# Performance work log

Measured on AMD Instinct MI355X. Metric: run time of the kernel, lower is better.

The kernel has to match this reference:

```python
import jax, jax.numpy as jnp
import numpy as np

RADIUS = 0.2
N_POINT = 1024   # FPS centroids
N_SAMPLE = 64    # ball-query neighbors


def swish(x):
    return x * jax.nn.sigmoid(x)


def farthest_point_sample(xyz, npoint):
    # xyz: [B, N, 3] -> [B, npoint] int32 indices (deterministic: start = arange(B) % N)
    B, N, _ = xyz.shape
    batch = jnp.arange(B)

    def step(carry, _):
        distance, farthest = carry
        centroid = xyz[batch, farthest][:, None, :]            # [B,1,3]
        dist = jnp.sum((xyz - centroid) ** 2, axis=-1)          # [B,N]
        distance = jnp.minimum(distance, dist)
        nxt = jnp.argmax(distance, axis=-1).astype(jnp.int32)
        return (distance, nxt), farthest

    init = (jnp.full((B, N), 1e10, dtype=xyz.dtype),
            (jnp.arange(B, dtype=jnp.int32) % N))
    _, idx = jax.lax.scan(step, init, None, length=npoint)      # [npoint, B]
    return idx.T                                                # [B, npoint]


def square_distance(src, dst):
    # src [B,S,3], dst [B,N,3] -> [B,S,N]
    return (jnp.sum(src ** 2, -1)[:, :, None]
            + jnp.sum(dst ** 2, -1)[:, None, :]
            - 2.0 * jnp.einsum('bsc,bnc->bsn', src, dst))


def query_ball_point(radius, nsample, xyz, new_xyz):
    # xyz [B,N,3], new_xyz [B,S,3] -> [B,S,nsample] int32
    N = xyz.shape[1]
    sqrdists = square_distance(new_xyz, xyz)                     # [B,S,N]
    arange_n = jnp.arange(N, dtype=jnp.int32)
    group_idx = jnp.where(sqrdists > radius ** 2, N, arange_n[None, None, :])
    group_idx = jnp.sort(group_idx, axis=-1)[:, :, :nsample]     # [B,S,K]
    first = group_idx[:, :, :1]
    return jnp.where(group_idx == N, first, group_idx).astype(jnp.int32)


def index_points(points, idx):
    # points [B,N,C], idx [B,...] -> [B,...,C]
    return jax.vmap(lambda p, i: p[i])(points, idx)


def setup_inputs() -> dict:
    key = jax.random.key(0)
    k1, k2, k3, k4 = jax.random.split(key, 4)
    B, N, D = 4, 16384, 256
    c_in = D + 3  # 259
    xyz = jax.random.normal(k1, (B, 3, N), dtype=jnp.float32)
    points = jax.random.normal(k2, (B, D, N), dtype=jnp.float32)
    w1 = jax.random.normal(k3, (512, c_in), dtype=jnp.float32) / np.sqrt(c_in)
    b1 = jnp.zeros((512,), dtype=jnp.float32)
    w2 = jax.random.normal(k4, (512, 512), dtype=jnp.float32) / np.sqrt(512)
    b2 = jnp.zeros((512,), dtype=jnp.float32)
    return {"xyz": xyz, "points": points, "w1": w1, "b1": b1, "w2": w2, "b2": b2}


def reference(xyz, points, w1, b1, w2, b2):
    x = jnp.transpose(xyz, (0, 2, 1))        # [B,N,3]
    p = jnp.transpose(points, (0, 2, 1))     # [B,N,D]

    fps_idx = farthest_point_sample(x, N_POINT)                  # [B,S]
    new_xyz = index_points(x, fps_idx)                           # [B,S,3]
    idx = query_ball_point(RADIUS, N_SAMPLE, x, new_xyz)         # [B,S,K]
    grouped_xyz = index_points(x, idx)                           # [B,S,K,3]
    grouped_norm = grouped_xyz - new_xyz[:, :, None, :]
    grouped_pts = index_points(p, idx)                           # [B,S,K,D]
    feat = jnp.concatenate([grouped_norm, grouped_pts], axis=-1) # [B,S,K,3+D]

    h = jnp.transpose(feat, (0, 3, 2, 1))                        # [B,C,K,S]
    # 1x1 convs (patch_size=1) == per-position channel GEMM
    h = swish(jnp.einsum('bcks,oc->boks', h, w1) + b1[None, :, None, None])
    h = swish(jnp.einsum('bcks,oc->boks', h, w2) + b2[None, :, None, None])
    return jnp.mean(h, axis=2)                                   # [B,512,S]
```

## Files before the change

kernel.cpp:

```cpp
#include <hip/hip_runtime.h>
#include <hip/hip_bf16.h>
#include <stdint.h>

#define BB 4
#define NN 16384
#define SS 1024
#define KSAMP 64
#define DD 256
#define CIN 259
#define HH 512
#define R2C 0.04f

#define OFF_PTS  0ull
#define OFF_Q    33554432ull
#define OFF_W1P  33816576ull
#define OFF_W2P  34111488ull
#define OFF_CX   34635776ull
#define OFF_CY   34652160ull
#define OFF_CZ   34668544ull
#define OFF_BIDX 34684928ull

typedef __attribute__((ext_vector_type(8))) short bf16x8;
typedef __attribute__((ext_vector_type(4))) short bf16x4;
typedef __attribute__((ext_vector_type(4))) float f32x4;

__device__ __forceinline__ unsigned short f2bf(float f) {
    unsigned u = __float_as_uint(f);
    u = u + 0x7fffu + ((u >> 16) & 1u);
    return (unsigned short)(u >> 16);
}

__global__ __launch_bounds__(1024) void k_prep(const float* __restrict__ xyz,
                                               const float* __restrict__ pts,
                                               const float* __restrict__ w1,
                                               const float* __restrict__ w2,
                                               unsigned char* __restrict__ ws)
{
    __shared__ __align__(16) unsigned char smem[64 * 264 * 2];
    const int blk = blockIdx.x;
    const int t   = threadIdx.x;

    if (blk < 4) {
        const int b = blk;
        const float* xb = xyz + (size_t)b * 3 * NN;
        float x[16], y[16], z[16], d[16];
        const int base = t * 16;
        const float4* xv = (const float4*)(xb + base);
        const float4* yv = (const float4*)(xb + NN + base);
        const float4* zv = (const float4*)(xb + 2 * NN + base);
#pragma unroll
        for (int i = 0; i < 4; i++) {
            float4 a = xv[i]; x[4*i]=a.x; x[4*i+1]=a.y; x[4*i+2]=a.z; x[4*i+3]=a.w;
            float4 c = yv[i]; y[4*i]=c.x; y[4*i+1]=c.y; y[4*i+2]=c.z; y[4*i+3]=c.w;
            float4 e = zv[i]; z[4*i]=e.x; z[4*i+1]=e.y; z[4*i+2]=e.z; z[4*i+3]=e.w;
        }
#pragma unroll
        for (int i = 0; i < 16; i++) d[i] = 1e10f;

        float* sC    = (float*)smem;
        float* sWMax = (float*)smem + 4;
        int*   sWin  = (int*)((float*)smem + 20);
        float* cxs = (float*)(ws + OFF_CX);
        float* cys = (float*)(ws + OFF_CY);
        float* czs = (float*)(ws + OFF_CZ);

        if (t == (b >> 4)) {
#pragma unroll
            for (int k = 0; k < 16; k++)
                if ((b & 15) == k) { sC[0] = x[k]; sC[1] = y[k]; sC[2] = z[k]; }
        }
        __syncthreads();

        for (int it = 0; it < SS; ++it) {
            const float cx = sC[0], cy = sC[1], cz = sC[2];
            if (t == 0) {
                cxs[(b << 10) + it] = cx;
                cys[(b << 10) + it] = cy;
                czs[(b << 10) + it] = cz;
                *sWin = 0x7fffffff;
            }
            if (it == SS - 1) break;

            float bl = -1.0f;
#pragma unroll
            for (int k = 0; k < 16; k++) {
                float dx = __fsub_rn(x[k], cx);
                float dy = __fsub_rn(y[k], cy);
                float dz = __fsub_rn(z[k], cz);
                float s  = __fadd_rn(__fadd_rn(__fmul_rn(dx, dx), __fmul_rn(dy, dy)),
                                     __fmul_rn(dz, dz));
                float nd = fminf(d[k], s);
                d[k] = nd;
                bl = fmaxf(bl, nd);
            }
            float bm = bl;
#pragma unroll
            for (int off = 32; off; off >>= 1) bm = fmaxf(bm, __shfl_xor(bm, off));
            if ((t & 63) == 0) sWMax[t >> 6] = bm;
            __syncthreads();

            float gm = sWMax[0];
#pragma unroll
            for (int wv = 1; wv < 16; wv++) gm = fmaxf(gm, sWMax[wv]);

            if (bl == gm) {
                int cand = 0x7fffffff;
#pragma unroll
                for (int k = 15; k >= 0; k--) if (d[k] == gm) cand = base + k;
                atomicMin(sWin, cand);
            }
            __syncthreads();
            const int w = *sWin;
            if (t == (w >> 4)) {
                const int wk = w & 15;
#pragma unroll
                for (int k = 0; k < 16; k++)
                    if (wk == k) { sC[0] = x[k]; sC[1] = y[k]; sC[2] = z[k]; }
            }
            __syncthreads();
        }
    } else if (blk < 1028) {
        const int tb = blk - 4;
        const int b  = tb >> 8;
        const int n0 = (tb & 255) << 6;
        unsigned short* sT = (unsigned short*)smem;
        const int tn = t & 63, tc = t >> 6;
        for (int cc = tc; cc < 256; cc += 16) {
            float v = pts[((size_t)(b * 256 + cc)) * NN + n0 + tn];
            sT[tn * 264 + cc] = f2bf(v);
        }
        __syncthreads();
        unsigned short* ptsT = (unsigned short*)(ws + OFF_PTS);
        const int r = t >> 4, part = t & 15;
        size_t ob = (((size_t)b * NN) + n0 + r) * 256 + part * 16;
        bf16x8* dst = (bf16x8*)(ptsT + ob);
        const bf16x8* src = (const bf16x8*)(sT + r * 264 + part * 16);
        dst[0] = src[0];
        dst[1] = src[1];
    } else if (blk < 1092) {
        const int qb = blk - 1028;
        const int b = qb >> 4;
        const int n = ((qb & 15) << 10) + t;
        const float* xb = xyz + (size_t)b * 3 * NN;
        float X = xb[n], Y = xb[NN + n], Z = xb[2 * NN + n];
        float q = __fadd_rn(__fadd_rn(__fmul_rn(X, X), __fmul_rn(Y, Y)), __fmul_rn(Z, Z));
        ((float*)(ws + OFF_Q))[b * NN + n] = q;
    } else if (blk == 1092) {
        unsigned short* w1p = (unsigned short*)(ws + OFF_W1P);
        for (int e = t; e < 32 * 9 * 64 * 8; e += 1024) {
            int j = e & 7, lane = (e >> 3) & 63, rest = e >> 9;
            int kt = rest % 9, nt = rest / 9;
            int kk = kt * 32 + 4 * (lane >> 4) + (j & 3) + 16 * (j >> 2);
            int o  = nt * 16 + (lane & 15);
            float v = 0.f;
            if (kk < CIN) {
                int c = (kk < 256) ? (kk + 3) : (kk - 256);
                v = w1[o * CIN + c];
            }
            w1p[e] = f2bf(v);
        }
    } else if (blk == 1093) {
        unsigned short* w2p = (unsigned short*)(ws + OFF_W2P);
        for (int e = t; e < 32 * 16 * 64 * 8; e += 1024) {
            int j = e & 7, lane = (e >> 3) & 63, rest = e >> 9;
            int kt = rest & 15, nt = rest >> 4;
            int kk = kt * 32 + 4 * (lane >> 4) + (j & 3) + 16 * (j >> 2);
            int o  = nt * 16 + (lane & 15);
            w2p[e] = f2bf(w2[o * 512 + kk]);
        }
    }
}

__global__ __launch_bounds__(256) void k_ball(const float* __restrict__ xyz,
                                              unsigned char* __restrict__ ws)
{
    const int s    = (blockIdx.x << 2) + (threadIdx.x >> 6);
    const int lane = threadIdx.x & 63;
    const int b    = s >> 10;
    const float* Q  = (const float*)(ws + OFF_Q) + b * NN;
    const float cx = ((const float*)(ws + OFF_CX))[s];
    const float cy = ((const float*)(ws + OFF_CY))[s];
    const float cz = ((const float*)(ws + OFF_CZ))[s];
    const float qc = __fadd_rn(__fadd_rn(__fmul_rn(cx, cx), __fmul_rn(cy, cy)),
                               __fmul_rn(cz, cz));
    const float* xb = xyz + (size_t)b * 3 * NN;
    int* gi = (int*)(ws + OFF_BIDX) + s * 64;

    int collected = 0;
    int first = -1;
    for (int c = 0; c < 256; c++) {
        const int n = (c << 6) + lane;
        float px = xb[n], py = xb[NN + n], pz = xb[2 * NN + n], qj = Q[n];
        float dot = __fadd_rn(__fadd_rn(__fmul_rn(cx, px), __fmul_rn(cy, py)),
                              __fmul_rn(cz, pz));
        float r = __fsub_rn(__fadd_rn(qc, qj), __fmul_rn(2.0f, dot));
        bool valid = !(r > R2C);
        unsigned long long m = __ballot(valid);
        if (m) {
            if (first < 0) first = (c << 6) + __builtin_ctzll(m);
            int rank = __popcll(m & ((1ull << lane) - 1ull));
            int slot = collected + rank;
            if (valid && slot < 64) gi[slot] = n;
            collected += __popcll(m);
            if (collected >= 64) break;
        }
    }
    if (collected < 64) {
        for (int k = collected + lane; k < 64; k += 64) gi[k] = first;
    }
}

__global__ __launch_bounds__(512) void k_mlp(const float* __restrict__ xyz,
                                             const float* __restrict__ b1,
                                             const float* __restrict__ b2,
                                             const unsigned char* __restrict__ ws,
                                             float* __restrict__ out)
{
    __shared__ __align__(16) unsigned short sFeat[64 * 296];
    __shared__ __align__(16) unsigned short sH1[64 * 520];
    __shared__ int sIdx[64];

    const int sblk = blockIdx.x;
    const int b = sblk >> 10, sq = sblk & 1023;
    const int t = threadIdx.x;

    const int* gi = (const int*)(ws + OFF_BIDX) + sblk * 64;
    if (t < 64) sIdx[t] = gi[t];
    __syncthreads();

    {
        const unsigned short* ptsT = (const unsigned short*)(ws + OFF_PTS);
        const int k = t >> 3, part = t & 7;
        const int n = sIdx[k];
        const bf16x8* src = (const bf16x8*)(ptsT + (((size_t)b * NN + n) * 256 + part * 32));
        bf16x8* dst = (bf16x8*)(sFeat + k * 296 + part * 32);
#pragma unroll
        for (int j = 0; j < 4; j++) dst[j] = src[j];
    }
    if (t < 64) {
        const int n = sIdx[t];
        const float* xb = xyz + (size_t)b * 3 * NN;
        const float cx = ((const float*)(ws + OFF_CX))[sblk];
        const float cy = ((const float*)(ws + OFF_CY))[sblk];
        const float cz = ((const float*)(ws + OFF_CZ))[sblk];
        sFeat[t * 296 + 256] = f2bf(__fsub_rn(xb[n], cx));
        sFeat[t * 296 + 257] = f2bf(__fsub_rn(xb[NN + n], cy));
        sFeat[t * 296 + 258] = f2bf(__fsub_rn(xb[2 * NN + n], cz));
#pragma unroll
        for (int c = 259; c < 288; c++) sFeat[t * 296 + c] = 0;
    }
    __syncthreads();

    const int wv = t >> 6, lane = t & 63;
    const int l15 = lane & 15, g = lane >> 4;

    f32x4 acc[4][4];
#pragma unroll
    for (int i = 0; i < 4; i++)
#pragma unroll
        for (int j = 0; j < 4; j++) acc[i][j] = (f32x4){0.f, 0.f, 0.f, 0.f};

    const bf16x8* w1v = (const bf16x8*)(ws + OFF_W1P);
    for (int kt = 0; kt < 9; kt++) {
        bf16x8 af[4];
#pragma unroll
        for (int mt = 0; mt < 4; mt++) {
            const unsigned short* p = sFeat + (mt * 16 + l15) * 296 + kt * 32 + 4 * g;
            bf16x4 lo = *(const bf16x4*)p;
            bf16x4 hi = *(const bf16x4*)(p + 16);
            af[mt] = __builtin_shufflevector(lo, hi, 0, 1, 2, 3, 4, 5, 6, 7);
        }
        bf16x8 bfr[4];
#pragma unroll
        for (int nti = 0; nti < 4; nti++)
            bfr[nti] = w1v[((wv * 4 + nti) * 9 + kt) * 64 + lane];
#pragma unroll
        for (int mt = 0; mt < 4; mt++)
#pragma unroll
            for (int nti = 0; nti < 4; nti++)
                acc[mt][nti] = __builtin_amdgcn_mfma_f32_16x16x32_bf16(
                    af[mt], bfr[nti], acc[mt][nti], 0, 0, 0);
    }
#pragma unroll
    for (int mt = 0; mt < 4; mt++)
#pragma unroll
        for (int nti = 0; nti < 4; nti++) {
            const int o = (wv * 4 + nti) * 16 + l15;
            const float bias = b1[o];
#pragma unroll
            for (int r = 0; r < 4; r++) {
                float v = acc[mt][nti][r] + bias;
                float sw = v / (1.f + __expf(-v));
                sH1[(mt * 16 + g * 4 + r) * 520 + o] = f2bf(sw);
            }
        }
    __syncthreads();

#pragma unroll
    for (int i = 0; i < 4; i++)
#pragma unroll
        for (int j = 0; j < 4; j++) acc[i][j] = (f32x4){0.f, 0.f, 0.f, 0.f};

    const bf16x8* w2v = (const bf16x8*)(ws + OFF_W2P);
    for (int kt = 0; kt < 16; kt++) {
        bf16x8 af[4];
#pragma unroll
        for (int mt = 0; mt < 4; mt++) {
            const unsigned short* p = sH1 + (mt * 16 + l15) * 520 + kt * 32 + 4 * g;
            bf16x4 lo = *(const bf16x4*)p;
            bf16x4 hi = *(const bf16x4*)(p + 16);
            af[mt] = __builtin_shufflevector(lo, hi, 0, 1, 2, 3, 4, 5, 6, 7);
        }
        bf16x8 bfr[4];
#pragma unroll
        for (int nti = 0; nti < 4; nti++)
            bfr[nti] = w2v[((wv * 4 + nti) * 16 + kt) * 64 + lane];
#pragma unroll
        for (int mt = 0; mt < 4; mt++)
#pragma unroll
            for (int nti = 0; nti < 4; nti++)
                acc[mt][nti] = __builtin_amdgcn_mfma_f32_16x16x32_bf16(
                    af[mt], bfr[nti], acc[mt][nti], 0, 0, 0);
    }
#pragma unroll
    for (int nti = 0; nti < 4; nti++) {
        float tot = 0.f;
        const int o = (wv * 4 + nti) * 16 + l15;
        const float bias = b2[o];
#pragma unroll
        for (int mt = 0; mt < 4; mt++) {
#pragma unroll
            for (int r = 0; r < 4; r++) {
                float v = acc[mt][nti][r] + bias;
                tot += v / (1.f + __expf(-v));
            }
        }
        tot += __shfl_xor(tot, 16);
        tot += __shfl_xor(tot, 32);
        if (lane < 16) {
            const int oo = (wv * 4 + nti) * 16 + lane;
            out[((size_t)b * 512 + oo) * 1024 + sq] = tot * 0.015625f;
        }
    }
}

extern "C" void kernel_launch(void* const* d_in, const int* in_sizes, int n_in,
                              void* d_out, int out_size, void* d_ws, size_t ws_size,
                              hipStream_t stream)
{
    const float* xyz = (const float*)d_in[0];
    const float* pts = (const float*)d_in[1];
    const float* w1  = (const float*)d_in[2];
    const float* b1  = (const float*)d_in[3];
    const float* w2  = (const float*)d_in[4];
    const float* b2  = (const float*)d_in[5];
    float* out = (float*)d_out;
    unsigned char* ws = (unsigned char*)d_ws;

    k_prep<<<1094, 1024, 0, stream>>>(xyz, pts, w1, w2, ws);
    k_ball<<<1024, 256, 0, stream>>>(xyz, ws);
    k_mlp<<<4096, 512, 0, stream>>>(xyz, b1, b2, ws, out);
}
```

Measured before the change: 1.901 ms.

## Cut FPS barriers using packed max-index keys and fewer threads

The farthest-point-sampling loop now packs the distance and inverted index into a 64-bit key and reduces it with wavefront shuffles, which needs one block barrier per iteration instead of three. A double-buffered shared slot lets that single barrier suffice, and every thread reads the winning centroid straight from global memory. The prep kernel drops to 512 threads so each thread covers 32 points, shrinking the cross-wave reduction to 8 waves. The other prep roles are adjusted to the new thread count. The trade-off is more registers per thread and a dependent global load on each serial FPS iteration.

```diff
diff --git a/kernel.cpp b/kernel.cpp
--- a/kernel.cpp
+++ b/kernel.cpp
@@ -30,11 +30,11 @@
     return (unsigned short)(u >> 16);
 }
 
-__global__ __launch_bounds__(1024) void k_prep(const float* __restrict__ xyz,
-                                               const float* __restrict__ pts,
-                                               const float* __restrict__ w1,
-                                               const float* __restrict__ w2,
-                                               unsigned char* __restrict__ ws)
+__global__ __launch_bounds__(512) void k_prep(const float* __restrict__ xyz,
+                                              const float* __restrict__ pts,
+                                              const float* __restrict__ w1,
+                                              const float* __restrict__ w2,
+                                              unsigned char* __restrict__ ws)
 {
     __shared__ __align__(16) unsigned char smem[64 * 264 * 2];
     const int blk = blockIdx.x;
@@ -43,47 +43,40 @@
     if (blk < 4) {
         const int b = blk;
         const float* xb = xyz + (size_t)b * 3 * NN;
-        float x[16], y[16], z[16], d[16];
-        const int base = t * 16;
+        float x[32], y[32], z[32], d[32];
+        const int base = t * 32;
         const float4* xv = (const float4*)(xb + base);
         const float4* yv = (const float4*)(xb + NN + base);
         const float4* zv = (const float4*)(xb + 2 * NN + base);
 #pragma unroll
-        for (int i = 0; i < 4; i++) {
+        for (int i = 0; i < 8; i++) {
             float4 a = xv[i]; x[4*i]=a.x; x[4*i+1]=a.y; x[4*i+2]=a.z; x[4*i+3]=a.w;
             float4 c = yv[i]; y[4*i]=c.x; y[4*i+1]=c.y; y[4*i+2]=c.z; y[4*i+3]=c.w;
             float4 e = zv[i]; z[4*i]=e.x; z[4*i+1]=e.y; z[4*i+2]=e.z; z[4*i+3]=e.w;
         }
 #pragma unroll
-        for (int i = 0; i < 16; i++) d[i] = 1e10f;
-
-        float* sC    = (float*)smem;
-        float* sWMax = (float*)smem + 4;
-        int*   sWin  = (int*)((float*)smem + 20);
+        for (int i = 0; i < 32; i++) d[i] = 1e10f;
+
+        unsigned long long* sK = (unsigned long long*)smem;
         float* cxs = (float*)(ws + OFF_CX);
         float* cys = (float*)(ws + OFF_CY);
         float* czs = (float*)(ws + OFF_CZ);
 
-        if (t == (b >> 4)) {
-#pragma unroll
-            for (int k = 0; k < 16; k++)
-                if ((b & 15) == k) { sC[0] = x[k]; sC[1] = y[k]; sC[2] = z[k]; }
-        }
-        __syncthreads();
+        const int wv = t >> 6, lane = t & 63;
+        float cx = xb[b], cy = xb[NN + b], cz = xb[2 * NN + b];
 
         for (int it = 0; it < SS; ++it) {
-            const float cx = sC[0], cy = sC[1], cz = sC[2];
             if (t == 0) {
                 cxs[(b << 10) + it] = cx;
                 cys[(b << 10) + it] = cy;
                 czs[(b << 10) + it] = cz;
-                *sWin = 0x7fffffff;
             }
             if (it == SS - 1) break;
 
             float bl = -1.0f;
-#pragma unroll
-            for (int k = 0; k < 16; k++) {
+            int   bi = 0;
+#pragma unroll
+            for (int k = 0; k < 32; k++) {
                 float dx = __fsub_rn(x[k], cx);
                 float dy = __fsub_rn(y[k], cy);
                 float dz = __fsub_rn(z[k], cz);
@@ -91,63 +84,63 @@
                                      __fmul_rn(dz, dz));
                 float nd = fminf(d[k], s);
                 d[k] = nd;
-                bl = fmaxf(bl, nd);
-            }
-            float bm = bl;
-#pragma unroll
-            for (int off = 32; off; off >>= 1) bm = fmaxf(bm, __shfl_xor(bm, off));
-            if ((t & 63) == 0) sWMax[t >> 6] = bm;
+                if (nd > bl) { bl = nd; bi = base + k; }
+            }
+            unsigned long long key =
+                ((unsigned long long)__float_as_uint(bl) << 32) |
+                (unsigned)(0xFFFFFFFFu - (unsigned)bi);
+#pragma unroll
+            for (int off = 1; off < 64; off <<= 1) {
+                unsigned long long o = __shfl_xor(key, off);
+                if (o > key) key = o;
+            }
+            if (lane == 0) sK[((it & 1) << 3) + wv] = key;
             __syncthreads();
 
-            float gm = sWMax[0];
-#pragma unroll
-            for (int wv = 1; wv < 16; wv++) gm = fmaxf(gm, sWMax[wv]);
-
-            if (bl == gm) {
-                int cand = 0x7fffffff;
-#pragma unroll
-                for (int k = 15; k >= 0; k--) if (d[k] == gm) cand = base + k;
-                atomicMin(sWin, cand);
-            }
-            __syncthreads();
-            const int w = *sWin;
-            if (t == (w >> 4)) {
-                const int wk = w & 15;
-#pragma unroll
-                for (int k = 0; k < 16; k++)
-                    if (wk == k) { sC[0] = x[k]; sC[1] = y[k]; sC[2] = z[k]; }
-            }
-            __syncthreads();
+            unsigned long long gk = sK[((it & 1) << 3) + (lane & 7)];
+#pragma unroll
+            for (int off = 1; off < 8; off <<= 1) {
+                unsigned long long o = __shfl_xor(gk, off);
+                if (o > gk) gk = o;
+            }
+            const int widx = (int)(0xFFFFFFFFu - (unsigned)gk);
+            cx = xb[widx]; cy = xb[NN + widx]; cz = xb[2 * NN + widx];
         }
     } else if (blk < 1028) {
         const int tb = blk - 4;
         const int b  = tb >> 8;
         const int n0 = (tb & 255) << 6;
         unsigned short* sT = (unsigned short*)smem;
-        const int tn = t & 63, tc = t >> 6;
-        for (int cc = tc; cc < 256; cc += 16) {
+        const int tn = t & 63, tc0 = t >> 6;
+        for (int cc = tc0; cc < 256; cc += 8) {
             float v = pts[((size_t)(b * 256 + cc)) * NN + n0 + tn];
             sT[tn * 264 + cc] = f2bf(v);
         }
         __syncthreads();
         unsigned short* ptsT = (unsigned short*)(ws + OFF_PTS);
-        const int r = t >> 4, part = t & 15;
-        size_t ob = (((size_t)b * NN) + n0 + r) * 256 + part * 16;
+        const int r = t >> 3, part = t & 7;
+        size_t ob = (((size_t)b * NN) + n0 + r) * 256 + part * 32;
         bf16x8* dst = (bf16x8*)(ptsT + ob);
-        const bf16x8* src = (const bf16x8*)(sT + r * 264 + part * 16);
+        const bf16x8* src = (const bf16x8*)(sT + r * 264 + part * 32);
         dst[0] = src[0];
         dst[1] = src[1];
+        dst[2] = src[2];
+        dst[3] = src[3];
     } else if (blk < 1092) {
         const int qb = blk - 1028;
         const int b = qb >> 4;
-        const int n = ((qb & 15) << 10) + t;
+        const int n0 = (qb & 15) << 10;
         const float* xb = xyz + (size_t)b * 3 * NN;
-        float X = xb[n], Y = xb[NN + n], Z = xb[2 * NN + n];
-        float q = __fadd_rn(__fadd_rn(__fmul_rn(X, X), __fmul_rn(Y, Y)), __fmul_rn(Z, Z));
-        ((float*)(ws + OFF_Q))[b * NN + n] = q;
+#pragma unroll
+        for (int i = 0; i < 2; i++) {
+            const int n = n0 + t + i * 512;
+            float X = xb[n], Y = xb[NN + n], Z = xb[2 * NN + n];
+            float q = __fadd_rn(__fadd_rn(__fmul_rn(X, X), __fmul_rn(Y, Y)), __fmul_rn(Z, Z));
+            ((float*)(ws + OFF_Q))[b * NN + n] = q;
+        }
     } else if (blk == 1092) {
         unsigned short* w1p = (unsigned short*)(ws + OFF_W1P);
-        for (int e = t; e < 32 * 9 * 64 * 8; e += 1024) {
+        for (int e = t; e < 32 * 9 * 64 * 8; e += 512) {
             int j = e & 7, lane = (e >> 3) & 63, rest = e >> 9;
             int kt = rest % 9, nt = rest / 9;
             int kk = kt * 32 + 4 * (lane >> 4) + (j & 3) + 16 * (j >> 2);
@@ -161,7 +154,7 @@
         }
     } else if (blk == 1093) {
         unsigned short* w2p = (unsigned short*)(ws + OFF_W2P);
-        for (int e = t; e < 32 * 16 * 64 * 8; e += 1024) {
+        for (int e = t; e < 32 * 16 * 64 * 8; e += 512) {
             int j = e & 7, lane = (e >> 3) & 63, rest = e >> 9;
             int kt = rest & 15, nt = rest >> 4;
             int kk = kt * 32 + 4 * (lane >> 4) + (j & 3) + 16 * (j >> 2);
@@ -357,7 +350,7 @@
     float* out = (float*)d_out;
     unsigned char* ws = (unsigned char*)d_ws;
 
-    k_prep<<<1094, 1024, 0, stream>>>(xyz, pts, w1, w2, ws);
+    k_prep<<<1094, 512, 0, stream>>>(xyz, pts, w1, w2, ws);
     k_ball<<<1024, 256, 0, stream>>>(xyz, ws);
     k_mlp<<<4096, 512, 0, stream>>>(xyz, b1, b2, ws, out);
 }
```

New measurement: 2.322 ms. +22.1%, slower.

## Overlap FPS with ball query and MLP via progress-flag streaming in fused kernel

Applied to the files above, without the earlier changes.

Moves farthest point sampling out of the prep kernel into the first four blocks of a new fused kernel. Those blocks publish centroids and a per-batch progress counter with release stores. The remaining blocks spin on the counter, then run the ball query and the two-layer MLP for their centroid, so the serial FPS loop overlaps with downstream work instead of finishing before it starts. The fused blocks use 1024 threads with 2 N-tiles per wave instead of 512 threads with 4, and the ball-index buffer becomes shared memory. The risk is deadlock if the FPS blocks are not scheduled before the waiting blocks, plus polling overhead and lower occupancy from the larger shared-memory footprint.

```diff
diff --git a/kernel.cpp b/kernel.cpp
--- a/kernel.cpp
+++ b/kernel.cpp
@@ -18,7 +18,7 @@
 #define OFF_CX   34635776ull
 #define OFF_CY   34652160ull
 #define OFF_CZ   34668544ull
-#define OFF_BIDX 34684928ull
+#define OFF_PROG 34684928ull
 
 typedef __attribute__((ext_vector_type(8))) short bf16x8;
 typedef __attribute__((ext_vector_type(4))) short bf16x4;
@@ -30,99 +30,19 @@
     return (unsigned short)(u >> 16);
 }
 
-__global__ __launch_bounds__(1024) void k_prep(const float* __restrict__ xyz,
-                                               const float* __restrict__ pts,
-                                               const float* __restrict__ w1,
-                                               const float* __restrict__ w2,
-                                               unsigned char* __restrict__ ws)
+__global__ __launch_bounds__(1024) void k_prep2(const float* __restrict__ xyz,
+                                                const float* __restrict__ pts,
+                                                const float* __restrict__ w1,
+                                                const float* __restrict__ w2,
+                                                unsigned char* __restrict__ ws)
 {
     __shared__ __align__(16) unsigned char smem[64 * 264 * 2];
     const int blk = blockIdx.x;
     const int t   = threadIdx.x;
 
-    if (blk < 4) {
-        const int b = blk;
-        const float* xb = xyz + (size_t)b * 3 * NN;
-        float x[16], y[16], z[16], d[16];
-        const int base = t * 16;
-        const float4* xv = (const float4*)(xb + base);
-        const float4* yv = (const float4*)(xb + NN + base);
-        const float4* zv = (const float4*)(xb + 2 * NN + base);
-#pragma unroll
-        for (int i = 0; i < 4; i++) {
-            float4 a = xv[i]; x[4*i]=a.x; x[4*i+1]=a.y; x[4*i+2]=a.z; x[4*i+3]=a.w;
-            float4 c = yv[i]; y[4*i]=c.x; y[4*i+1]=c.y; y[4*i+2]=c.z; y[4*i+3]=c.w;
-            float4 e = zv[i]; z[4*i]=e.x; z[4*i+1]=e.y; z[4*i+2]=e.z; z[4*i+3]=e.w;
-        }
-#pragma unroll
-        for (int i = 0; i < 16; i++) d[i] = 1e10f;
-
-        float* sC    = (float*)smem;
-        float* sWMax = (float*)smem + 4;
-        int*   sWin  = (int*)((float*)smem + 20);
-        float* cxs = (float*)(ws + OFF_CX);
-        float* cys = (float*)(ws + OFF_CY);
-        float* czs = (float*)(ws + OFF_CZ);
-
-        if (t == (b >> 4)) {
-#pragma unroll
-            for (int k = 0; k < 16; k++)
-                if ((b & 15) == k) { sC[0] = x[k]; sC[1] = y[k]; sC[2] = z[k]; }
-        }
-        __syncthreads();
-
-        for (int it = 0; it < SS; ++it) {
-            const float cx = sC[0], cy = sC[1], cz = sC[2];
-            if (t == 0) {
-                cxs[(b << 10) + it] = cx;
-                cys[(b << 10) + it] = cy;
-                czs[(b << 10) + it] = cz;
-                *sWin = 0x7fffffff;
-            }
-            if (it == SS - 1) break;
-
-            float bl = -1.0f;
-#pragma unroll
-            for (int k = 0; k < 16; k++) {
-                float dx = __fsub_rn(x[k], cx);
-                float dy = __fsub_rn(y[k], cy);
-                float dz = __fsub_rn(z[k], cz);
-                float s  = __fadd_rn(__fadd_rn(__fmul_rn(dx, dx), __fmul_rn(dy, dy)),
-                                     __fmul_rn(dz, dz));
-                float nd = fminf(d[k], s);
-                d[k] = nd;
-                bl = fmaxf(bl, nd);
-            }
-            float bm = bl;
-#pragma unroll
-            for (int off = 32; off; off >>= 1) bm = fmaxf(bm, __shfl_xor(bm, off));
-            if ((t & 63) == 0) sWMax[t >> 6] = bm;
-            __syncthreads();
-
-            float gm = sWMax[0];
-#pragma unroll
-            for (int wv = 1; wv < 16; wv++) gm = fmaxf(gm, sWMax[wv]);
-
-            if (bl == gm) {
-                int cand = 0x7fffffff;
-#pragma unroll
-                for (int k = 15; k >= 0; k--) if (d[k] == gm) cand = base + k;
-                atomicMin(sWin, cand);
-            }
-            __syncthreads();
-            const int w = *sWin;
-            if (t == (w >> 4)) {
-                const int wk = w & 15;
-#pragma unroll
-                for (int k = 0; k < 16; k++)
-                    if (wk == k) { sC[0] = x[k]; sC[1] = y[k]; sC[2] = z[k]; }
-            }
-            __syncthreads();
-        }
-    } else if (blk < 1028) {
-        const int tb = blk - 4;
-        const int b  = tb >> 8;
-        const int n0 = (tb & 255) << 6;
+    if (blk < 1024) {
+        const int b  = blk >> 8;
+        const int n0 = (blk & 255) << 6;
         unsigned short* sT = (unsigned short*)smem;
         const int tn = t & 63, tc = t >> 6;
         for (int cc = tc; cc < 256; cc += 16) {
@@ -137,15 +57,15 @@
         const bf16x8* src = (const bf16x8*)(sT + r * 264 + part * 16);
         dst[0] = src[0];
         dst[1] = src[1];
-    } else if (blk < 1092) {
-        const int qb = blk - 1028;
+    } else if (blk < 1088) {
+        const int qb = blk - 1024;
         const int b = qb >> 4;
         const int n = ((qb & 15) << 10) + t;
         const float* xb = xyz + (size_t)b * 3 * NN;
         float X = xb[n], Y = xb[NN + n], Z = xb[2 * NN + n];
         float q = __fadd_rn(__fadd_rn(__fmul_rn(X, X), __fmul_rn(Y, Y)), __fmul_rn(Z, Z));
         ((float*)(ws + OFF_Q))[b * NN + n] = q;
-    } else if (blk == 1092) {
+    } else if (blk == 1088) {
         unsigned short* w1p = (unsigned short*)(ws + OFF_W1P);
         for (int e = t; e < 32 * 9 * 64 * 8; e += 1024) {
             int j = e & 7, lane = (e >> 3) & 63, rest = e >> 9;
@@ -159,7 +79,7 @@
             }
             w1p[e] = f2bf(v);
         }
-    } else if (blk == 1093) {
+    } else {
         unsigned short* w2p = (unsigned short*)(ws + OFF_W2P);
         for (int e = t; e < 32 * 16 * 64 * 8; e += 1024) {
             int j = e & 7, lane = (e >> 3) & 63, rest = e >> 9;
@@ -171,78 +91,172 @@
     }
 }
 
-__global__ __launch_bounds__(256) void k_ball(const float* __restrict__ xyz,
-                                              unsigned char* __restrict__ ws)
+__global__ __launch_bounds__(1024) void k_fused(const float* __restrict__ xyz,
+                                                const float* __restrict__ b1,
+                                                const float* __restrict__ b2,
+                                                unsigned char* __restrict__ ws,
+                                                float* __restrict__ out)
 {
-    const int s    = (blockIdx.x << 2) + (threadIdx.x >> 6);
-    const int lane = threadIdx.x & 63;
-    const int b    = s >> 10;
-    const float* Q  = (const float*)(ws + OFF_Q) + b * NN;
-    const float cx = ((const float*)(ws + OFF_CX))[s];
-    const float cy = ((const float*)(ws + OFF_CY))[s];
-    const float cz = ((const float*)(ws + OFF_CZ))[s];
-    const float qc = __fadd_rn(__fadd_rn(__fmul_rn(cx, cx), __fmul_rn(cy, cy)),
-                               __fmul_rn(cz, cz));
+    __shared__ __align__(16) unsigned char smem[104832];
+    const int blk = blockIdx.x;
+    const int t   = threadIdx.x;
+    int* prog = (int*)(ws + OFF_PROG);
+    float* cxs = (float*)(ws + OFF_CX);
+    float* cys = (float*)(ws + OFF_CY);
+    float* czs = (float*)(ws + OFF_CZ);
+
+    if (blk < 4) {
+        const int b = blk;
+        const float* xb = xyz + (size_t)b * 3 * NN;
+        float x[16], y[16], z[16], d[16];
+        const int base = t * 16;
+        const float4* xv = (const float4*)(xb + base);
+        const float4* yv = (const float4*)(xb + NN + base);
+        const float4* zv = (const float4*)(xb + 2 * NN + base);
+#pragma unroll
+        for (int i = 0; i < 4; i++) {
+            float4 a = xv[i]; x[4*i]=a.x; x[4*i+1]=a.y; x[4*i+2]=a.z; x[4*i+3]=a.w;
+            float4 c = yv[i]; y[4*i]=c.x; y[4*i+1]=c.y; y[4*i+2]=c.z; y[4*i+3]=c.w;
+            float4 e = zv[i]; z[4*i]=e.x; z[4*i+1]=e.y; z[4*i+2]=e.z; z[4*i+3]=e.w;
+        }
+#pragma unroll
+        for (int i = 0; i < 16; i++) d[i] = 1e10f;
+
+        float* sC    = (float*)smem;
+        float* sWMax = (float*)smem + 4;
+        int*   sWin  = (int*)((float*)smem + 20);
+
+        if (t == (b >> 4)) {
+#pragma unroll
+            for (int k = 0; k < 16; k++)
+                if ((b & 15) == k) { sC[0] = x[k]; sC[1] = y[k]; sC[2] = z[k]; }
+        }
+        __syncthreads();
+
+        for (int it = 0; it < SS; ++it) {
+            const float cx = sC[0], cy = sC[1], cz = sC[2];
+            if (t == 0) {
+                __hip_atomic_store(&cxs[(b << 10) + it], cx, __ATOMIC_RELAXED,
+                                   __HIP_MEMORY_SCOPE_AGENT);
+                __hip_atomic_store(&cys[(b << 10) + it], cy, __ATOMIC_RELAXED,
+                                   __HIP_MEMORY_SCOPE_AGENT);
+                __hip_atomic_store(&czs[(b << 10) + it], cz, __ATOMIC_RELAXED,
+                                   __HIP_MEMORY_SCOPE_AGENT);
+                if ((it & 7) == 0)
+                    __hip_atomic_store(&prog[b], it, __ATOMIC_RELEASE,
+                                       __HIP_MEMORY_SCOPE_AGENT);
+                *sWin = 0x7fffffff;
+            }
+            if (it == SS - 1) break;
+
+            float bl = -1.0f;
+#pragma unroll
+            for (int k = 0; k < 16; k++) {
+                float dx = __fsub_rn(x[k], cx);
+                float dy = __fsub_rn(y[k], cy);
+                float dz = __fsub_rn(z[k], cz);
+                float s  = __fadd_rn(__fadd_rn(__fmul_rn(dx, dx), __fmul_rn(dy, dy)),
+                                     __fmul_rn(dz, dz));
+                float nd = fminf(d[k], s);
+                d[k] = nd;
+                bl = fmaxf(bl, nd);
+            }
+            float bm = bl;
+#pragma unroll
+            for (int off = 32; off; off >>= 1) bm = fmaxf(bm, __shfl_xor(bm, off));
+            if ((t & 63) == 0) sWMax[t >> 6] = bm;
+            __syncthreads();
+
+            float gm = sWMax[0];
+#pragma unroll
+            for (int wv = 1; wv < 16; wv++) gm = fmaxf(gm, sWMax[wv]);
+
+            if (bl == gm) {
+                int cand = 0x7fffffff;
+#pragma unroll
+                for (int k = 15; k >= 0; k--) if (d[k] == gm) cand = base + k;
+                atomicMin(sWin, cand);
+            }
+            __syncthreads();
+            const int w = *sWin;
+            if (t == (w >> 4)) {
+                const int wk = w & 15;
+#pragma unroll
+                for (int k = 0; k < 16; k++)
+                    if (wk == k) { sC[0] = x[k]; sC[1] = y[k]; sC[2] = z[k]; }
+            }
+            __syncthreads();
+        }
+        if (t == 0)
+            __hip_atomic_store(&prog[b], SS, __ATOMIC_RELEASE,
+                               __HIP_MEMORY_SCOPE_AGENT);
+        return;
+    }
+
+    const int i = blk - 4;
+    const int b = i & 3, s = i >> 2;
+    const int cs = (b << 10) + s;
+
+    unsigned short* sFeat = (unsigned short*)smem;
+    unsigned short* sH1   = (unsigned short*)(smem + 37888);
+    int*            sIdx  = (int*)(smem + 104448);
+
+    if (t == 0) {
+        while (__hip_atomic_load(&prog[b], __ATOMIC_ACQUIRE,
+                                 __HIP_MEMORY_SCOPE_AGENT) <= s)
+            __builtin_amdgcn_s_sleep(8);
+    }
+    __syncthreads();
+
+    const float cx = __hip_atomic_load(&cxs[cs], __ATOMIC_RELAXED,
+                                       __HIP_MEMORY_SCOPE_AGENT);
+    const float cy = __hip_atomic_load(&cys[cs], __ATOMIC_RELAXED,
+                                       __HIP_MEMORY_SCOPE_AGENT);
+    const float cz = __hip_atomic_load(&czs[cs], __ATOMIC_RELAXED,
+                                       __HIP_MEMORY_SCOPE_AGENT);
     const float* xb = xyz + (size_t)b * 3 * NN;
-    int* gi = (int*)(ws + OFF_BIDX) + s * 64;
-
-    int collected = 0;
-    int first = -1;
-    for (int c = 0; c < 256; c++) {
-        const int n = (c << 6) + lane;
-        float px = xb[n], py = xb[NN + n], pz = xb[2 * NN + n], qj = Q[n];
-        float dot = __fadd_rn(__fadd_rn(__fmul_rn(cx, px), __fmul_rn(cy, py)),
-                              __fmul_rn(cz, pz));
-        float r = __fsub_rn(__fadd_rn(qc, qj), __fmul_rn(2.0f, dot));
-        bool valid = !(r > R2C);
-        unsigned long long m = __ballot(valid);
-        if (m) {
-            if (first < 0) first = (c << 6) + __builtin_ctzll(m);
-            int rank = __popcll(m & ((1ull << lane) - 1ull));
-            int slot = collected + rank;
-            if (valid && slot < 64) gi[slot] = n;
-            collected += __popcll(m);
-            if (collected >= 64) break;
-        }
-    }
-    if (collected < 64) {
-        for (int k = collected + lane; k < 64; k += 64) gi[k] = first;
-    }
-}
-
-__global__ __launch_bounds__(512) void k_mlp(const float* __restrict__ xyz,
-                                             const float* __restrict__ b1,
-                                             const float* __restrict__ b2,
-                                             const unsigned char* __restrict__ ws,
-                                             float* __restrict__ out)
-{
-    __shared__ __align__(16) unsigned short sFeat[64 * 296];
-    __shared__ __align__(16) unsigned short sH1[64 * 520];
-    __shared__ int sIdx[64];
-
-    const int sblk = blockIdx.x;
-    const int b = sblk >> 10, sq = sblk & 1023;
-    const int t = threadIdx.x;
-
-    const int* gi = (const int*)(ws + OFF_BIDX) + sblk * 64;
-    if (t < 64) sIdx[t] = gi[t];
+
+    if (t < 64) {
+        const int lane = t;
+        const float* Q = (const float*)(ws + OFF_Q) + b * NN;
+        const float qc = __fadd_rn(__fadd_rn(__fmul_rn(cx, cx), __fmul_rn(cy, cy)),
+                                   __fmul_rn(cz, cz));
+        int collected = 0;
+        int first = -1;
+        for (int c = 0; c < 256; c++) {
+            const int n = (c << 6) + lane;
+            float px = xb[n], py = xb[NN + n], pz = xb[2 * NN + n], qj = Q[n];
+            float dot = __fadd_rn(__fadd_rn(__fmul_rn(cx, px), __fmul_rn(cy, py)),
+                                  __fmul_rn(cz, pz));
+            float r = __fsub_rn(__fadd_rn(qc, qj), __fmul_rn(2.0f, dot));
+            bool valid = !(r > R2C);
+            unsigned long long m = __ballot(valid);
+            if (m) {
+                if (first < 0) first = (c << 6) + __builtin_ctzll(m);
+                int rank = __popcll(m & ((1ull << lane) - 1ull));
+                int slot = collected + rank;
+                if (valid && slot < 64) sIdx[slot] = n;
+                collected += __popcll(m);
+                if (collected >= 64) break;
+            }
+        }
+        if (collected < 64) {
+            for (int k = collected + lane; k < 64; k += 64) sIdx[k] = first;
+        }
+    }
     __syncthreads();
 
     {
         const unsigned short* ptsT = (const unsigned short*)(ws + OFF_PTS);
-        const int k = t >> 3, part = t & 7;
+        const int k = t >> 4, part = t & 15;
         const int n = sIdx[k];
-        const bf16x8* src = (const bf16x8*)(ptsT + (((size_t)b * NN + n) * 256 + part * 32));
-        bf16x8* dst = (bf16x8*)(sFeat + k * 296 + part * 32);
-#pragma unroll
-        for (int j = 0; j < 4; j++) dst[j] = src[j];
+        const bf16x8* src = (const bf16x8*)(ptsT + ((size_t)b * NN + n) * 256 + part * 16);
+        bf16x8* dst = (bf16x8*)(sFeat + k * 296 + part * 16);
+        dst[0] = src[0];
+        dst[1] = src[1];
     }
     if (t < 64) {
         const int n = sIdx[t];
-        const float* xb = xyz + (size_t)b * 3 * NN;
-        const float cx = ((const float*)(ws + OFF_CX))[sblk];
-        const float cy = ((const float*)(ws + OFF_CY))[sblk];
-        const float cz = ((const float*)(ws + OFF_CZ))[sblk];
         sFeat[t * 296 + 256] = f2bf(__fsub_rn(xb[n], cx));
         sFeat[t * 296 + 257] = f2bf(__fsub_rn(xb[NN + n], cy));
         sFeat[t * 296 + 258] = f2bf(__fsub_rn(xb[2 * NN + n], cz));
@@ -254,11 +268,11 @@
     const int wv = t >> 6, lane = t & 63;
     const int l15 = lane & 15, g = lane >> 4;
 
-    f32x4 acc[4][4];
-#pragma unroll
-    for (int i = 0; i < 4; i++)
-#pragma unroll
-        for (int j = 0; j < 4; j++) acc[i][j] = (f32x4){0.f, 0.f, 0.f, 0.f};
+    f32x4 acc[4][2];
+#pragma unroll
+    for (int a = 0; a < 4; a++)
+#pragma unroll
+        for (int j = 0; j < 2; j++) acc[a][j] = (f32x4){0.f, 0.f, 0.f, 0.f};
 
     const bf16x8* w1v = (const bf16x8*)(ws + OFF_W1P);
     for (int kt = 0; kt < 9; kt++) {
@@ -270,22 +284,22 @@
             bf16x4 hi = *(const bf16x4*)(p + 16);
             af[mt] = __builtin_shufflevector(lo, hi, 0, 1, 2, 3, 4, 5, 6, 7);
         }
-        bf16x8 bfr[4];
-#pragma unroll
-        for (int nti = 0; nti < 4; nti++)
-            bfr[nti] = w1v[((wv * 4 + nti) * 9 + kt) * 64 + lane];
+        bf16x8 bfr[2];
+#pragma unroll
+        for (int nti = 0; nti < 2; nti++)
+            bfr[nti] = w1v[((wv * 2 + nti) * 9 + kt) * 64 + lane];
 #pragma unroll
         for (int mt = 0; mt < 4; mt++)
 #pragma unroll
-            for (int nti = 0; nti < 4; nti++)
+            for (int nti = 0; nti < 2; nti++)
                 acc[mt][nti] = __builtin_amdgcn_mfma_f32_16x16x32_bf16(
                     af[mt], bfr[nti], acc[mt][nti], 0, 0, 0);
     }
 #pragma unroll
     for (int mt = 0; mt < 4; mt++)
 #pragma unroll
-        for (int nti = 0; nti < 4; nti++) {
-            const int o = (wv * 4 + nti) * 16 + l15;
+        for (int nti = 0; nti < 2; nti++) {
+            const int o = (wv * 2 + nti) * 16 + l15;
             const float bias = b1[o];
 #pragma unroll
             for (int r = 0; r < 4; r++) {
@@ -297,9 +311,9 @@
     __syncthreads();
 
 #pragma unroll
-    for (int i = 0; i < 4; i++)
-#pragma unroll
-        for (int j = 0; j < 4; j++) acc[i][j] = (f32x4){0.f, 0.f, 0.f, 0.f};
+    for (int a = 0; a < 4; a++)
+#pragma unroll
+        for (int j = 0; j < 2; j++) acc[a][j] = (f32x4){0.f, 0.f, 0.f, 0.f};
 
     const bf16x8* w2v = (const bf16x8*)(ws + OFF_W2P);
     for (int kt = 0; kt < 16; kt++) {
@@ -311,21 +325,21 @@
             bf16x4 hi = *(const bf16x4*)(p + 16);
             af[mt] = __builtin_shufflevector(lo, hi, 0, 1, 2, 3, 4, 5, 6, 7);
         }
-        bf16x8 bfr[4];
-#pragma unroll
-        for (int nti = 0; nti < 4; nti++)
-            bfr[nti] = w2v[((wv * 4 + nti) * 16 + kt) * 64 + lane];
+        bf16x8 bfr[2];
+#pragma unroll
+        for (int nti = 0; nti < 2; nti++)
+            bfr[nti] = w2v[((wv * 2 + nti) * 16 + kt) * 64 + lane];
 #pragma unroll
         for (int mt = 0; mt < 4; mt++)
 #pragma unroll
-            for (int nti = 0; nti < 4; nti++)
+            for (int nti = 0; nti < 2; nti++)
                 acc[mt][nti] = __builtin_amdgcn_mfma_f32_16x16x32_bf16(
                     af[mt], bfr[nti], acc[mt][nti], 0, 0, 0);
     }
 #pragma unroll
-    for (int nti = 0; nti < 4; nti++) {
+    for (int nti = 0; nti < 2; nti++) {
         float tot = 0.f;
-        const int o = (wv * 4 + nti) * 16 + l15;
+        const int o = (wv * 2 + nti) * 16 + l15;
         const float bias = b2[o];
 #pragma unroll
         for (int mt = 0; mt < 4; mt++) {
@@ -338,8 +352,8 @@
         tot += __shfl_xor(tot, 16);
         tot += __shfl_xor(tot, 32);
         if (lane < 16) {
-            const int oo = (wv * 4 + nti) * 16 + lane;
-            out[((size_t)b * 512 + oo) * 1024 + sq] = tot * 0.015625f;
+            const int oo = (wv * 2 + nti) * 16 + lane;
+            out[((size_t)b * 512 + oo) * 1024 + s] = tot * 0.015625f;
         }
     }
 }
@@ -357,7 +371,7 @@
     float* out = (float*)d_out;
     unsigned char* ws = (unsigned char*)d_ws;
 
-    k_prep<<<1094, 1024, 0, stream>>>(xyz, pts, w1, w2, ws);
-    k_ball<<<1024, 256, 0, stream>>>(xyz, ws);
-    k_mlp<<<4096, 512, 0, stream>>>(xyz, b1, b2, ws, out);
+    hipMemsetAsync((void*)(ws + OFF_PROG), 0xFF, 16, stream);
+    k_prep2<<<1090, 1024, 0, stream>>>(xyz, pts, w1, w2, ws);
+    k_fused<<<4100, 1024, 0, stream>>>(xyz, b1, b2, ws, out);
 }
```

Result: faster. 1.647 ms, median of 2 (-13.4%).
